# Performance work log

Measured on AMD Instinct MI355X. Metric: run time of the kernel, lower is better.

Reference implementation:

```python
import jax, jax.numpy as jnp
import numpy as np
from jax import lax

STRIDES = (2, 2)
PADDING = 'same'  # matches init_kwargs


def _tconv_pad(k, s, padding):
    """Per-dim (lo, hi) padding so conv_general_dilated with lhs_dilation=s
    reproduces tf.nn.conv2d_transpose with the given padding mode."""
    if padding == 'valid':
        return (k - 1, k - 1)  # 'full' padding; out = (in-1)*s + k
    pt_fwd = max(k - s, 0) // 2          # top pad of the corresponding forward SAME conv
    pb = k - 1 - pt_fwd
    pa = (k + s - 2) - pb                # total transpose pad = k + s - 2; out = in*s
    return (pb, pa)


def setup_inputs() -> dict:
    key = jax.random.key(0)
    k_in, k_dw, k_pw = jax.random.split(key, 3)
    B, H, W, C = 16, 64, 64, 256
    KH = KW = 4
    D = 1          # depth_multiplier
    F = 256        # filters
    inputs = jax.random.normal(k_in, (B, H, W, C), dtype=jnp.float32)
    dw_kernel = jax.random.normal(k_dw, (KH, KW, C, D), dtype=jnp.float32) * 0.05
    pw_kernel = jax.random.normal(k_pw, (1, 1, C * D, F), dtype=jnp.float32) * 0.05
    bias = jnp.zeros((F,), dtype=jnp.float32)
    return {"inputs": inputs, "dw_kernel": dw_kernel, "pw_kernel": pw_kernel, "bias": bias}


def reference(inputs, dw_kernel, pw_kernel, bias):
    # Depthwise transposed conv. The original builds a dense (k,k,Cin*D,Cin)
    # kernel with an identity mask; mathematically that equals a grouped
    # transposed conv with groups=Cin, implemented here as a lhs-dilated
    # grouped conv with the spatially flipped depthwise kernel.
    kh, kw, cin, dm = dw_kernel.shape
    sh, sw = STRIDES
    # HWIO with I=1, O=cin*dm (channel order c*dm + d matches the masked-dense kernel)
    ker = jnp.flip(dw_kernel, (0, 1)).reshape(kh, kw, 1, cin * dm)
    pad = (_tconv_pad(kh, sh, PADDING), _tconv_pad(kw, sw, PADDING))
    x = lax.conv_general_dilated(
        inputs, ker,
        window_strides=(1, 1), padding=pad, lhs_dilation=(sh, sw),
        dimension_numbers=('NHWC', 'HWIO', 'NHWC'),
        feature_group_count=cin)  # [B, H*sh, W*sw, cin*dm] for SAME
    # 1x1 pointwise conv + bias + relu (fused elementwise tail)
    pw = pw_kernel[0, 0]                         # (cin*dm, filters)
    x = jnp.einsum('bhwc,cf->bhwf', x, pw)
    return jax.nn.relu(x + bias)
```

## Files before the change

### kernel.cpp

```cpp
#include <hip/hip_runtime.h>
#include <hip/hip_bf16.h>

#define BB 16
#define HH 64
#define WW 64
#define CC 256
#define OH 128
#define OW 128
#define FF 256

typedef __attribute__((ext_vector_type(8))) short bf16x8;
typedef __attribute__((ext_vector_type(4))) float f32x4;

__device__ __forceinline__ short f2bf(float x) {
    union { float f; unsigned u; } v; v.f = x;
    unsigned r = v.u + 0x7fffu + ((v.u >> 16) & 1u);
    return (short)(r >> 16);
}

__device__ __forceinline__ unsigned cvtpk(float lo, float hi) {
    unsigned r;
    asm("v_cvt_pk_bf16_f32 %0, %1, %2" : "=v"(r) : "v"(lo), "v"(hi));
    return r;
}

__global__ void prep_kernel(const float* __restrict__ pw, short* __restrict__ pwtF) {
    const int e    = blockIdx.x * 256 + threadIdx.x;
    const int lane = e & 63;
    const int ni   = (e >> 6) & 3;
    const int kk   = (e >> 8) & 7;
    const int wc   = e >> 11;
    const int f    = wc * 64 + ni * 16 + (lane & 15);
    const int c0   = kk * 32 + (lane >> 4) * 8;
    bf16x8 v;
    #pragma unroll
    for (int j = 0; j < 8; ++j) v[j] = f2bf(pw[(size_t)(c0 + j) * FF + f]);
    reinterpret_cast<bf16x8*>(pwtF)[e] = v;
}

__global__ __launch_bounds__(512, 2)
void sepconvt_kernel(const float* __restrict__ X,
                     const float* __restrict__ dw,
                     const short* __restrict__ pwtF,
                     const float* __restrict__ bias,
                     float* __restrict__ out) {
    __shared__ __align__(16) char xraw[98304];
    __shared__ bf16x8 t_lds[2][32 * 32];

    const int tid  = threadIdx.x;
    const int wid  = tid >> 6;
    const int lane = tid & 63;
    const int blk  = blockIdx.x;
    const int oh = blk & (OH - 1);
    const int b  = blk >> 7;

    int r0, r1, i0, i1;
    if (oh & 1) { r0 = 0; i0 = (oh + 1) >> 1; r1 = 2; i1 = (oh - 1) >> 1; }
    else        { r0 = 1; i0 = oh >> 1;       r1 = 3; i1 = (oh >> 1) - 1; }
    const bool va0 = (unsigned)i0 < HH;
    const bool va1 = (unsigned)i1 < HH;

    if (wid < 4) {
        const int w  = wid;
        const int c4 = lane << 2;
        const float* Xr0 = X + (size_t)(b * HH + (va0 ? i0 : 0)) * WW * CC + c4;
        const float* Xr1 = X + (size_t)(b * HH + (va1 ? i1 : 0)) * WW * CC + c4;

        float4 wt[2][2][2];
        {
            const float4 z = {0.f, 0.f, 0.f, 0.f};
            #pragma unroll
            for (int r = 0; r < 2; ++r) {
                const int rr = r ? r1 : r0;
                const bool va = r ? va1 : va0;
                float4 s0 = *reinterpret_cast<const float4*>(dw + (rr * 4 + 0) * CC + c4);
                float4 s1 = *reinterpret_cast<const float4*>(dw + (rr * 4 + 1) * CC + c4);
                float4 s2 = *reinterpret_cast<const float4*>(dw + (rr * 4 + 2) * CC + c4);
                float4 s3 = *reinterpret_cast<const float4*>(dw + (rr * 4 + 3) * CC + c4);
                wt[r][0][0] = va ? s1 : z;
                wt[r][0][1] = va ? s3 : z;
                wt[r][1][0] = va ? s0 : z;
                wt[r][1][1] = va ? s2 : z;
            }
        }

        auto STAGE = [&](int q, int qb) {
            const int W0  = q * 32 + w * 8;
            const int jlo = (W0 >> 1) - 1;
            const int base = qb * 49152 + w * 12288;
            #pragma unroll
            for (int ci = 0; ci < 6; ++ci) {
                int j = jlo + ci;
                j = j < 0 ? 0 : (j > WW - 1 ? WW - 1 : j);
                __builtin_amdgcn_global_load_lds(
                    (const __attribute__((address_space(1))) unsigned*)(Xr0 + (size_t)j * CC),
                    (__attribute__((address_space(3))) unsigned*)(xraw + base + ci * 1024),
                    16, 0, 0);
                __builtin_amdgcn_global_load_lds(
                    (const __attribute__((address_space(1))) unsigned*)(Xr1 + (size_t)j * CC),
                    (__attribute__((address_space(3))) unsigned*)(xraw + base + 6144 + ci * 1024),
                    16, 0, 0);
            }
        };

        auto LC = [&](const char* xw, int ci, float4& x0, float4& x1) {
            x0 = *reinterpret_cast<const float4*>(xw + ci * 1024 + lane * 16);
            x1 = *reinterpret_cast<const float4*>(xw + 6144 + ci * 1024 + lane * 16);
        };

        auto EMIT = [&](int qb, int owl, int p,
                        const float4& xe0, const float4& xe1,
                        const float4& xo0, const float4& xo1) {
            const float4 we0 = wt[0][p][0], wo0 = wt[0][p][1];
            const float4 we1 = wt[1][p][0], wo1 = wt[1][p][1];
            float a0 = we0.x * xe0.x + wo0.x * xo0.x + we1.x * xe1.x + wo1.x * xo1.x;
            float a1 = we0.y * xe0.y + wo0.y * xo0.y + we1.y * xe1.y + wo1.y * xo1.y;
            float a2 = we0.z * xe0.z + wo0.z * xo0.z + we1.z * xe1.z + wo1.z * xo1.z;
            float a3 = we0.w * xe0.w + wo0.w * xo0.w + we1.w * xe1.w + wo1.w * xo1.w;
            unsigned* dst = reinterpret_cast<unsigned*>(
                reinterpret_cast<char*>(&t_lds[qb][0]) + owl * 512 +
                (((lane >> 1) ^ (owl & 7)) << 4) + ((lane & 1) << 3));
            dst[0] = cvtpk(a0, a1);
            dst[1] = cvtpk(a2, a3);
        };

        auto PRODUCE = [&](int q, int qb) {
            const char* xw = xraw + qb * 49152 + w * 12288;
            const int W0 = q * 32 + w * 8;
            const int o0 = w * 8;
            float4 xo0, xo1, xe0, xe1;
            LC(xw, 0, xo0, xo1);
            LC(xw, 1, xe0, xe1);
            if (W0 == 0) { xo0 = (float4){0,0,0,0}; xo1 = (float4){0,0,0,0}; }
            EMIT(qb, o0 + 0, 0, xe0, xe1, xo0, xo1);
            xo0 = xe0; xo1 = xe1; LC(xw, 2, xe0, xe1);
            EMIT(qb, o0 + 1, 1, xe0, xe1, xo0, xo1);
            EMIT(qb, o0 + 2, 0, xe0, xe1, xo0, xo1);
            xo0 = xe0; xo1 = xe1; LC(xw, 3, xe0, xe1);
            EMIT(qb, o0 + 3, 1, xe0, xe1, xo0, xo1);
            EMIT(qb, o0 + 4, 0, xe0, xe1, xo0, xo1);
            xo0 = xe0; xo1 = xe1; LC(xw, 4, xe0, xe1);
            EMIT(qb, o0 + 5, 1, xe0, xe1, xo0, xo1);
            EMIT(qb, o0 + 6, 0, xe0, xe1, xo0, xo1);
            xo0 = xe0; xo1 = xe1; LC(xw, 5, xe0, xe1);
            if (W0 == 120) { xe0 = (float4){0,0,0,0}; xe1 = (float4){0,0,0,0}; }
            EMIT(qb, o0 + 7, 1, xe0, xe1, xo0, xo1);
        };

        STAGE(0, 0);
        #pragma unroll
        for (int q = 0; q < 4; ++q) {
            if (q < 3) {
                STAGE(q + 1, (q + 1) & 1);
                asm volatile("s_waitcnt vmcnt(12)" ::: "memory");
            } else {
                asm volatile("s_waitcnt vmcnt(0)" ::: "memory");
            }
            __builtin_amdgcn_sched_barrier(0);
            PRODUCE(q, q & 1);
            asm volatile("s_waitcnt lgkmcnt(0)" ::: "memory");
            __builtin_amdgcn_sched_barrier(0);
            asm volatile("s_barrier" ::: "memory");
        }
    } else {
        const int wc  = wid - 4;
        const int lr  = lane & 15;
        const int lk8 = lane >> 4;
        const bf16x8* pvF = reinterpret_cast<const bf16x8*>(pwtF) + (size_t)wc * 2048 + lane;

        f32x4 bv[4];
        #pragma unroll
        for (int ni = 0; ni < 4; ++ni)
            bv[ni] = *reinterpret_cast<const f32x4*>(&bias[wc * 64 + ni * 16 + lk8 * 4]);

        #pragma unroll
        for (int q = 0; q < 4; ++q) {
            asm volatile("s_barrier" ::: "memory");
            __builtin_amdgcn_sched_barrier(0);
            const int qb = q & 1;

            f32x4 acc[2][4];
            #pragma unroll
            for (int mi = 0; mi < 2; ++mi)
                #pragma unroll
                for (int ni = 0; ni < 4; ++ni)
                    acc[mi][ni] = (f32x4){0.f, 0.f, 0.f, 0.f};

            #pragma unroll
            for (int kk = 0; kk < 8; ++kk) {
                const int kg = kk * 4 + lk8;
                bf16x8 af[2], bfr[4];
                #pragma unroll
                for (int mi = 0; mi < 2; ++mi) {
                    const int row = mi * 16 + lr;
                    af[mi] = t_lds[qb][row * 32 + (kg ^ (row & 7))];
                }
                #pragma unroll
                for (int ni = 0; ni < 4; ++ni)
                    bfr[ni] = pvF[(kk * 4 + ni) * 64];
                #pragma unroll
                for (int mi = 0; mi < 2; ++mi)
                    #pragma unroll
                    for (int ni = 0; ni < 4; ++ni)
                        acc[mi][ni] = __builtin_amdgcn_mfma_f32_16x16x32_bf16(
                            bfr[ni], af[mi], acc[mi][ni], 0, 0, 0);
            }

            float* obase = out + ((size_t)(b * OH + oh) * OW + q * 32) * FF;
            #pragma unroll
            for (int ni = 0; ni < 4; ++ni) {
                const int f0 = wc * 64 + ni * 16 + lk8 * 4;
                #pragma unroll
                for (int mi = 0; mi < 2; ++mi) {
                    const int ow = mi * 16 + lr;
                    f32x4 v = acc[mi][ni] + bv[ni];
                    v[0] = v[0] > 0.f ? v[0] : 0.f;
                    v[1] = v[1] > 0.f ? v[1] : 0.f;
                    v[2] = v[2] > 0.f ? v[2] : 0.f;
                    v[3] = v[3] > 0.f ? v[3] : 0.f;
                    *reinterpret_cast<f32x4*>(&obase[(size_t)ow * FF + f0]) = v;
                }
            }
        }
    }
}

extern "C" void kernel_launch(void* const* d_in, const int* in_sizes, int n_in,
                              void* d_out, int out_size, void* d_ws, size_t ws_size,
                              hipStream_t stream) {
    (void)in_sizes; (void)n_in; (void)out_size; (void)ws_size;
    const float* X    = (const float*)d_in[0];
    const float* dw   = (const float*)d_in[1];
    const float* pw   = (const float*)d_in[2];
    const float* bias = (const float*)d_in[3];
    float* out = (float*)d_out;
    short* pwtF = (short*)d_ws;

    prep_kernel<<<dim3(32), dim3(256), 0, stream>>>(pw, pwtF);
    sepconvt_kernel<<<dim3(BB * OH), dim3(512), 0, stream>>>(X, dw, pwtF, bias, out);
}
```

Measured before the change: 126.2 us.

## Pre-convert input to bf16 in prep kernel and halve LDS staging

The prep kernel now also converts the whole fp32 input tensor to bf16 in workspace. The main kernel stages bf16 rows through LDS, so the buffer is half the size and launch bounds rise to 4 blocks per CU. The depthwise producer is reorganised so each lane handles 8 channels and half-waves split across output columns. The gain depends on the extra full read-and-write pass over the input costing less than the halved reads and higher occupancy recover; rounding the input to bf16 before the depthwise step also adds error.

```diff
diff --git a/kernel.cpp b/kernel.cpp
--- a/kernel.cpp
+++ b/kernel.cpp
@@ -24,27 +24,49 @@
     return r;
 }
 
-__global__ void prep_kernel(const float* __restrict__ pw, short* __restrict__ pwtF) {
-    const int e    = blockIdx.x * 256 + threadIdx.x;
-    const int lane = e & 63;
-    const int ni   = (e >> 6) & 3;
-    const int kk   = (e >> 8) & 7;
-    const int wc   = e >> 11;
-    const int f    = wc * 64 + ni * 16 + (lane & 15);
-    const int c0   = kk * 32 + (lane >> 4) * 8;
-    bf16x8 v;
-    #pragma unroll
-    for (int j = 0; j < 8; ++j) v[j] = f2bf(pw[(size_t)(c0 + j) * FF + f]);
-    reinterpret_cast<bf16x8*>(pwtF)[e] = v;
-}
-
-__global__ __launch_bounds__(512, 2)
-void sepconvt_kernel(const float* __restrict__ X,
+__device__ __forceinline__ float bf2f(short s) {
+    union { unsigned u; float f; } v;
+    v.u = ((unsigned)(unsigned short)s) << 16;
+    return v.f;
+}
+
+__global__ void prep_kernel(const float* __restrict__ X, const float* __restrict__ pw,
+                            short* __restrict__ Xbf, short* __restrict__ pwtF) {
+    const int blk = blockIdx.x, tid = threadIdx.x;
+    if (blk < 2048) {
+        const float4* src = reinterpret_cast<const float4*>(X);
+        bf16x8* dst = reinterpret_cast<bf16x8*>(Xbf);
+        #pragma unroll
+        for (int k = 0; k < 4; ++k) {
+            const int v2 = blk * 2048 + k * 512 + tid * 2;
+            float4 a = src[v2], c = src[v2 + 1];
+            union { unsigned u[4]; bf16x8 v; } pk;
+            pk.u[0] = cvtpk(a.x, a.y); pk.u[1] = cvtpk(a.z, a.w);
+            pk.u[2] = cvtpk(c.x, c.y); pk.u[3] = cvtpk(c.z, c.w);
+            dst[v2 >> 1] = pk.v;
+        }
+    } else {
+        const int e    = (blk - 2048) * 256 + tid;
+        const int lane = e & 63;
+        const int ni   = (e >> 6) & 3;
+        const int kk   = (e >> 8) & 7;
+        const int wc   = e >> 11;
+        const int f    = wc * 64 + ni * 16 + (lane & 15);
+        const int c0   = kk * 32 + (lane >> 4) * 8;
+        bf16x8 v;
+        #pragma unroll
+        for (int j = 0; j < 8; ++j) v[j] = f2bf(pw[(size_t)(c0 + j) * FF + f]);
+        reinterpret_cast<bf16x8*>(pwtF)[e] = v;
+    }
+}
+
+__global__ __launch_bounds__(512, 4)
+void sepconvt_kernel(const short* __restrict__ Xbf,
                      const float* __restrict__ dw,
                      const short* __restrict__ pwtF,
                      const float* __restrict__ bias,
                      float* __restrict__ out) {
-    __shared__ __align__(16) char xraw[98304];
+    __shared__ __align__(16) char xraw[49152];
     __shared__ bf16x8 t_lds[2][32 * 32];
 
     const int tid  = threadIdx.x;
@@ -61,90 +83,89 @@
     const bool va1 = (unsigned)i1 < HH;
 
     if (wid < 4) {
-        const int w  = wid;
-        const int c4 = lane << 2;
-        const float* Xr0 = X + (size_t)(b * HH + (va0 ? i0 : 0)) * WW * CC + c4;
-        const float* Xr1 = X + (size_t)(b * HH + (va1 ? i1 : 0)) * WW * CC + c4;
-
-        float4 wt[2][2][2];
+        const int w   = wid;
+        const int grp = lane >> 5;
+        const int ch  = lane & 31;
+        const int c0  = ch << 3;
+
+        const size_t xrow0 = (size_t)(b * HH + (va0 ? i0 : 0)) * WW * CC;
+        const size_t xrow1 = (size_t)(b * HH + (va1 ? i1 : 0)) * WW * CC;
+        const size_t xrowS = grp ? xrow1 : xrow0;
+
+        float we0[8], wo0[8], we1[8], wo1[8];
         {
-            const float4 z = {0.f, 0.f, 0.f, 0.f};
-            #pragma unroll
-            for (int r = 0; r < 2; ++r) {
-                const int rr = r ? r1 : r0;
-                const bool va = r ? va1 : va0;
-                float4 s0 = *reinterpret_cast<const float4*>(dw + (rr * 4 + 0) * CC + c4);
-                float4 s1 = *reinterpret_cast<const float4*>(dw + (rr * 4 + 1) * CC + c4);
-                float4 s2 = *reinterpret_cast<const float4*>(dw + (rr * 4 + 2) * CC + c4);
-                float4 s3 = *reinterpret_cast<const float4*>(dw + (rr * 4 + 3) * CC + c4);
-                wt[r][0][0] = va ? s1 : z;
-                wt[r][0][1] = va ? s3 : z;
-                wt[r][1][0] = va ? s0 : z;
-                wt[r][1][1] = va ? s2 : z;
+            const int se = grp ? 0 : 1;
+            const int so = grp ? 2 : 3;
+            const float4* d4;
+            #pragma unroll
+            for (int h = 0; h < 2; ++h) {
+                d4 = reinterpret_cast<const float4*>(dw + (r0 * 4 + se) * CC + c0) + h;
+                float4 a = *d4;
+                we0[h*4+0]=a.x; we0[h*4+1]=a.y; we0[h*4+2]=a.z; we0[h*4+3]=a.w;
+                d4 = reinterpret_cast<const float4*>(dw + (r0 * 4 + so) * CC + c0) + h;
+                a = *d4;
+                wo0[h*4+0]=a.x; wo0[h*4+1]=a.y; wo0[h*4+2]=a.z; wo0[h*4+3]=a.w;
+                d4 = reinterpret_cast<const float4*>(dw + (r1 * 4 + se) * CC + c0) + h;
+                a = *d4;
+                we1[h*4+0]=a.x; we1[h*4+1]=a.y; we1[h*4+2]=a.z; we1[h*4+3]=a.w;
+                d4 = reinterpret_cast<const float4*>(dw + (r1 * 4 + so) * CC + c0) + h;
+                a = *d4;
+                wo1[h*4+0]=a.x; wo1[h*4+1]=a.y; wo1[h*4+2]=a.z; wo1[h*4+3]=a.w;
+            }
+            if (!va0) {
+                #pragma unroll
+                for (int e = 0; e < 8; ++e) { we0[e]=0.f; wo0[e]=0.f; }
+            }
+            if (!va1) {
+                #pragma unroll
+                for (int e = 0; e < 8; ++e) { we1[e]=0.f; wo1[e]=0.f; }
             }
         }
 
         auto STAGE = [&](int q, int qb) {
             const int W0  = q * 32 + w * 8;
             const int jlo = (W0 >> 1) - 1;
-            const int base = qb * 49152 + w * 12288;
+            const int base = qb * 24576 + w * 6144;
             #pragma unroll
             for (int ci = 0; ci < 6; ++ci) {
                 int j = jlo + ci;
                 j = j < 0 ? 0 : (j > WW - 1 ? WW - 1 : j);
                 __builtin_amdgcn_global_load_lds(
-                    (const __attribute__((address_space(1))) unsigned*)(Xr0 + (size_t)j * CC),
+                    (const __attribute__((address_space(1))) unsigned*)(Xbf + xrowS + (size_t)j * CC + c0),
                     (__attribute__((address_space(3))) unsigned*)(xraw + base + ci * 1024),
                     16, 0, 0);
-                __builtin_amdgcn_global_load_lds(
-                    (const __attribute__((address_space(1))) unsigned*)(Xr1 + (size_t)j * CC),
-                    (__attribute__((address_space(3))) unsigned*)(xraw + base + 6144 + ci * 1024),
-                    16, 0, 0);
             }
         };
 
-        auto LC = [&](const char* xw, int ci, float4& x0, float4& x1) {
-            x0 = *reinterpret_cast<const float4*>(xw + ci * 1024 + lane * 16);
-            x1 = *reinterpret_cast<const float4*>(xw + 6144 + ci * 1024 + lane * 16);
-        };
-
-        auto EMIT = [&](int qb, int owl, int p,
-                        const float4& xe0, const float4& xe1,
-                        const float4& xo0, const float4& xo1) {
-            const float4 we0 = wt[0][p][0], wo0 = wt[0][p][1];
-            const float4 we1 = wt[1][p][0], wo1 = wt[1][p][1];
-            float a0 = we0.x * xe0.x + wo0.x * xo0.x + we1.x * xe1.x + wo1.x * xo1.x;
-            float a1 = we0.y * xe0.y + wo0.y * xo0.y + we1.y * xe1.y + wo1.y * xo1.y;
-            float a2 = we0.z * xe0.z + wo0.z * xo0.z + we1.z * xe1.z + wo1.z * xo1.z;
-            float a3 = we0.w * xe0.w + wo0.w * xo0.w + we1.w * xe1.w + wo1.w * xo1.w;
-            unsigned* dst = reinterpret_cast<unsigned*>(
-                reinterpret_cast<char*>(&t_lds[qb][0]) + owl * 512 +
-                (((lane >> 1) ^ (owl & 7)) << 4) + ((lane & 1) << 3));
-            dst[0] = cvtpk(a0, a1);
-            dst[1] = cvtpk(a2, a3);
-        };
-
         auto PRODUCE = [&](int q, int qb) {
-            const char* xw = xraw + qb * 49152 + w * 12288;
+            const char* xw = xraw + qb * 24576 + w * 6144;
             const int W0 = q * 32 + w * 8;
             const int o0 = w * 8;
-            float4 xo0, xo1, xe0, xe1;
-            LC(xw, 0, xo0, xo1);
-            LC(xw, 1, xe0, xe1);
-            if (W0 == 0) { xo0 = (float4){0,0,0,0}; xo1 = (float4){0,0,0,0}; }
-            EMIT(qb, o0 + 0, 0, xe0, xe1, xo0, xo1);
-            xo0 = xe0; xo1 = xe1; LC(xw, 2, xe0, xe1);
-            EMIT(qb, o0 + 1, 1, xe0, xe1, xo0, xo1);
-            EMIT(qb, o0 + 2, 0, xe0, xe1, xo0, xo1);
-            xo0 = xe0; xo1 = xe1; LC(xw, 3, xe0, xe1);
-            EMIT(qb, o0 + 3, 1, xe0, xe1, xo0, xo1);
-            EMIT(qb, o0 + 4, 0, xe0, xe1, xo0, xo1);
-            xo0 = xe0; xo1 = xe1; LC(xw, 4, xe0, xe1);
-            EMIT(qb, o0 + 5, 1, xe0, xe1, xo0, xo1);
-            EMIT(qb, o0 + 6, 0, xe0, xe1, xo0, xo1);
-            xo0 = xe0; xo1 = xe1; LC(xw, 5, xe0, xe1);
-            if (W0 == 120) { xe0 = (float4){0,0,0,0}; xe1 = (float4){0,0,0,0}; }
-            EMIT(qb, o0 + 7, 1, xe0, xe1, xo0, xo1);
+            #pragma unroll
+            for (int k = 0; k < 4; ++k) {
+                const int jeL = k + 1 + grp;
+                const int joL = k + grp;
+                bf16x8 xe0 = *reinterpret_cast<const bf16x8*>(xw + jeL * 1024 + 0   + ch * 16);
+                bf16x8 xe1 = *reinterpret_cast<const bf16x8*>(xw + jeL * 1024 + 512 + ch * 16);
+                bf16x8 xo0 = *reinterpret_cast<const bf16x8*>(xw + joL * 1024 + 0   + ch * 16);
+                bf16x8 xo1 = *reinterpret_cast<const bf16x8*>(xw + joL * 1024 + 512 + ch * 16);
+                const bool kill_o = (W0 == 0   && k == 0 && grp == 0);
+                const bool kill_e = (W0 == 120 && k == 3 && grp == 1);
+                float a8[8];
+                #pragma unroll
+                for (int e = 0; e < 8; ++e) {
+                    const float fe0 = kill_e ? 0.f : bf2f(xe0[e]);
+                    const float fe1 = kill_e ? 0.f : bf2f(xe1[e]);
+                    const float fo0 = kill_o ? 0.f : bf2f(xo0[e]);
+                    const float fo1 = kill_o ? 0.f : bf2f(xo1[e]);
+                    a8[e] = we0[e]*fe0 + wo0[e]*fo0 + we1[e]*fe1 + wo1[e]*fo1;
+                }
+                union { unsigned u[4]; bf16x8 v; } pk;
+                pk.u[0] = cvtpk(a8[0], a8[1]); pk.u[1] = cvtpk(a8[2], a8[3]);
+                pk.u[2] = cvtpk(a8[4], a8[5]); pk.u[3] = cvtpk(a8[6], a8[7]);
+                const int owl = o0 + 2 * k + grp;
+                t_lds[qb][owl * 32 + (ch ^ (owl & 7))] = pk.v;
+            }
         };
 
         STAGE(0, 0);
@@ -152,7 +173,7 @@
         for (int q = 0; q < 4; ++q) {
             if (q < 3) {
                 STAGE(q + 1, (q + 1) & 1);
-                asm volatile("s_waitcnt vmcnt(12)" ::: "memory");
+                asm volatile("s_waitcnt vmcnt(6)" ::: "memory");
             } else {
                 asm volatile("s_waitcnt vmcnt(0)" ::: "memory");
             }
@@ -234,8 +255,10 @@
     const float* pw   = (const float*)d_in[2];
     const float* bias = (const float*)d_in[3];
     float* out = (float*)d_out;
-    short* pwtF = (short*)d_ws;
-
-    prep_kernel<<<dim3(32), dim3(256), 0, stream>>>(pw, pwtF);
-    sepconvt_kernel<<<dim3(BB * OH), dim3(512), 0, stream>>>(X, dw, pwtF, bias, out);
-}
+
+    short* Xbf  = (short*)d_ws;
+    short* pwtF = (short*)((char*)d_ws + 33554432);
+
+    prep_kernel<<<dim3(2080), dim3(256), 0, stream>>>(X, pw, Xbf, pwtF);
+    sepconvt_kernel<<<dim3(BB * OH), dim3(512), 0, stream>>>(Xbf, dw, pwtF, bias, out);
+}
```

Result: slower. 132.4 us (+4.9%).
